# Performance work log

Measured on AMD Instinct MI355X. Metric: run time of the kernel, lower is better.

The kernel has to match this reference:

```python
import jax, jax.numpy as jnp
import numpy as np

EMBED = 1024
HEADS = 16
HEAD_DIM = EMBED // HEADS
EPS = 1e-5  # torch LayerNorm default


def setup_inputs() -> dict:
    key = jax.random.key(0)
    ks = jax.random.split(key, 11)
    s = 1.0 / np.sqrt(EMBED)
    def lin(kw, kb):
        W = jax.random.uniform(kw, (EMBED, EMBED), jnp.float32, -s, s)
        b = jax.random.uniform(kb, (EMBED,), jnp.float32, -s, s)
        return W, b
    Wq, bq = lin(ks[0], ks[1])
    Wk, bk = lin(ks[2], ks[3])
    Wv, bv = lin(ks[4], ks[5])
    Wo, bo = lin(ks[6], ks[7])
    x = jax.random.normal(ks[8], (2, 2048, EMBED), jnp.float32)
    gamma = jnp.ones((EMBED,), jnp.float32)
    beta = jnp.zeros((EMBED,), jnp.float32)
    return {"x": x, "Wq": Wq, "bq": bq, "Wk": Wk, "bk": bk,
            "Wv": Wv, "bv": bv, "Wo": Wo, "bo": bo,
            "gamma": gamma, "beta": beta}


def _attn(x, Wq, bq, Wk, bk, Wv, bv, Wo, bo, gamma, beta):
    N, S, _ = x.shape
    # torch Linear: y = x @ W.T + b
    q = (x @ Wq.T + bq).reshape(N, S, HEADS, HEAD_DIM).transpose(0, 2, 1, 3)
    k = (x @ Wk.T + bk).reshape(N, S, HEADS, HEAD_DIM).transpose(0, 2, 1, 3)
    v = (x @ Wv.T + bv).reshape(N, S, HEADS, HEAD_DIM).transpose(0, 2, 1, 3)
    energy = jnp.einsum("bhqd,bhkd->bhqk", q, k) / np.sqrt(HEAD_DIM)
    causal = jnp.tril(jnp.ones((S, S), bool))  # [S,S]
    energy = jnp.where(causal[None, None], energy, -jnp.inf)
    attn = jax.nn.softmax(energy, axis=-1)
    out = jnp.einsum("bhqk,bhkd->bhqd", attn, v)
    out = out.transpose(0, 2, 1, 3).reshape(N, S, EMBED)
    out = out @ Wo.T + bo
    # residual + LayerNorm
    h = out + x
    mu = jnp.mean(h, axis=-1, keepdims=True)
    var = jnp.var(h, axis=-1, keepdims=True)
    return (h - mu) * jax.lax.rsqrt(var + EPS) * gamma + beta


def reference(x, Wq, bq, Wk, bk, Wv, bv, Wo, bo, gamma, beta):
    return _attn(x, Wq, bq, Wk, bk, Wv, bv, Wo, bo, gamma, beta)
```

## Files before the change

kernel.cpp:

```cpp
#include <hip/hip_runtime.h>

typedef __attribute__((ext_vector_type(8))) short short8;
typedef __attribute__((ext_vector_type(4))) float f32x4;
typedef __attribute__((ext_vector_type(4))) short short4v;

__device__ __forceinline__ short f2bs(float f) {
    union { float f; unsigned u; } c; c.f = f;
    unsigned r = 0x7FFFu + ((c.u >> 16) & 1u);
    return (short)((c.u + r) >> 16);
}

__device__ __forceinline__ unsigned fbits(float f) {
    union { float f; unsigned u; } c; c.f = f; return c.u;
}

__device__ __forceinline__ float fast_exp2(float x) {
    float r;
    asm("v_exp_f32 %0, %1" : "=v"(r) : "v"(x));
    return r;
}

__device__ __forceinline__ void gld_lds16(const void* g, void* l) {
    __builtin_amdgcn_global_load_lds(
        (const __attribute__((address_space(1))) unsigned int*)g,
        (__attribute__((address_space(3))) unsigned int*)l, 16, 0, 0);
}

__device__ __forceinline__ f32x4 mfma16(short8 a, short8 b, f32x4 c) {
    return __builtin_amdgcn_mfma_f32_16x16x32_bf16(a, b, c, 0, 0, 0);
}

template<int N> __device__ __forceinline__ void vmwait() {
    if constexpr (N == 0)      asm volatile("s_waitcnt vmcnt(0)" ::: "memory");
    else if constexpr (N == 3) asm volatile("s_waitcnt vmcnt(3)" ::: "memory");
    else if constexpr (N == 4) asm volatile("s_waitcnt vmcnt(4)" ::: "memory");
}

__global__ __launch_bounds__(256) void cvtall_kernel(
    const float* __restrict__ x,
    const float* __restrict__ Wq, const float* __restrict__ Wk,
    const float* __restrict__ Wv, const float* __restrict__ Wo,
    short* __restrict__ xb, short* __restrict__ wqkv, short* __restrict__ wob)
{
    int i = blockIdx.x * 256 + threadIdx.x;
    const float* src; short* dst; int off;
    if (i < 1048576) { src = x; dst = xb; off = i; }
    else {
        int j = i - 1048576, which = j >> 18;
        off = j & 262143;
        src = which == 0 ? Wq : (which == 1 ? Wk : (which == 2 ? Wv : Wo));
        dst = which == 3 ? wob : (wqkv + (size_t)which * 1048576);
    }
    float4 v = ((const float4*)src)[off];
    short4v o;
    o.x = f2bs(v.x); o.y = f2bs(v.y); o.z = f2bs(v.z); o.w = f2bs(v.w);
    ((short4v*)dst)[off] = o;
}

#define BN 128
#define BK 32

template<int MODE, int BMt>
__global__ __launch_bounds__(256) void gemm_bt(
    const short* __restrict__ A, const short* __restrict__ B,
    int M, int N, int K,
    const float* __restrict__ b0, const float* __restrict__ b1, const float* __restrict__ b2,
    short* __restrict__ oq, short* __restrict__ ok_, short* __restrict__ ov,
    const float* __restrict__ bo, const float* __restrict__ xres,
    float* __restrict__ outf)
{
    constexpr int IM = BMt / 32;
    constexpr int BUFSZ = (BMt + BN) * BK;
    constexpr int LPS = (BMt == 128) ? 4 : 3;
    __shared__ __align__(16) short SM[3 * BUFSZ];
    const int tid = threadIdx.x;
    const int wave = tid >> 6, lane = tid & 63;
    const int lhi = lane >> 4, llo = lane & 15;
    const int row0 = blockIdx.x * BMt, col0 = blockIdx.y * BN;
    const int wr = (wave >> 1) * (BMt / 2), wc = (wave & 1) * 64;

    f32x4 acc[IM][4] = {};

    const short* gA0 = A + (size_t)(row0 + (tid >> 2)) * K + (tid & 3) * 8;
    const short* gA1 = A + (size_t)(row0 + 64 + (tid >> 2)) * K + (tid & 3) * 8;
    const short* gB0 = B + (size_t)(col0 + (tid >> 2)) * K + (tid & 3) * 8;
    const short* gB1 = B + (size_t)(col0 + 64 + (tid >> 2)) * K + (tid & 3) * 8;

    auto stage = [&](int kk, int bf) {
        short* As = SM + bf * BUFSZ;
        short* Bs = As + BMt * BK;
        gld_lds16(gA0 + kk, &As[wave * 512]);
        if constexpr (BMt == 128) gld_lds16(gA1 + kk, &As[2048 + wave * 512]);
        gld_lds16(gB0 + kk, &Bs[wave * 512]);
        gld_lds16(gB1 + kk, &Bs[2048 + wave * 512]);
    };

    const int NT = K / BK;
    stage(0, 0);
    stage(BK, 1);

    for (int kt = 0; kt < NT; ++kt) {
        if (kt < NT - 1) vmwait<LPS>(); else vmwait<0>();
        __builtin_amdgcn_s_barrier();
        __builtin_amdgcn_sched_barrier(0);
        if (kt + 2 < NT) stage((kt + 2) * BK, (kt + 2) % 3);
        const short* As = SM + (kt % 3) * BUFSZ;
        const short* Bs = As + BMt * BK;
        short8 af[IM], bfr[4];
        #pragma unroll
        for (int i = 0; i < IM; ++i)
            af[i] = *(const short8*)&As[(wr + i * 16 + llo) * BK + lhi * 8];
        #pragma unroll
        for (int j = 0; j < 4; ++j)
            bfr[j] = *(const short8*)&Bs[(wc + j * 16 + llo) * BK + lhi * 8];
        #pragma unroll
        for (int i = 0; i < IM; ++i)
            #pragma unroll
            for (int j = 0; j < 4; ++j)
                acc[i][j] = mfma16(af[i], bfr[j], acc[i][j]);
    }

    if constexpr (MODE == 0) {
        const int which = (int)blockIdx.y >> 3;
        if (which < 2) {
            const float* bia = which == 0 ? b0 : b1;
            short* dst = which == 0 ? oq : ok_;
            #pragma unroll
            for (int i = 0; i < IM; ++i)
                #pragma unroll
                for (int j = 0; j < 4; ++j)
                    #pragma unroll
                    for (int r = 0; r < 4; ++r) {
                        int m = row0 + wr + i * 16 + lhi * 4 + r;
                        int nn = (col0 & 1023) + wc + j * 16 + llo;
                        float v = acc[i][j][r] + bia[nn];
                        int h = nn >> 6, d = nn & 63;
                        int bb = m >> 11, s = m & 2047;
                        dst[((size_t)((bb * 16 + h) * 2048 + s)) * 64 + d] = f2bs(v);
                    }
        } else {
            __syncthreads();
            short* T = SM + wave * (64 * 26);
            const int nn0 = (col0 - 2048) + wc;
            const int h = nn0 >> 6;
            const int bb = row0 >> 11;
            const int s0 = (row0 & 2047) + wr;
            short* vdst = ov + ((size_t)(bb * 16 + h) * 64) * 2048;
            #pragma unroll
            for (int i = 0; i < IM; ++i) {
                #pragma unroll
                for (int j = 0; j < 4; ++j) {
                    const float bias = b2[nn0 + j * 16 + llo];
                    unsigned u01 = __builtin_amdgcn_perm(fbits(acc[i][j][1] + bias),
                                                         fbits(acc[i][j][0] + bias), 0x07060302u);
                    unsigned u23 = __builtin_amdgcn_perm(fbits(acc[i][j][3] + bias),
                                                         fbits(acc[i][j][2] + bias), 0x07060302u);
                    unsigned* Tw = (unsigned*)&T[(j * 16 + llo) * 26];
                    Tw[lhi * 2]     = u01;
                    Tw[lhi * 2 + 1] = u23;
                }
                short8 a0 = *(const short8*)&T[lane * 26];
                short8 a1 = *(const short8*)&T[lane * 26 + 8];
                *(short8*)&vdst[(size_t)lane * 2048 + s0 + i * 16]     = a0;
                *(short8*)&vdst[(size_t)lane * 2048 + s0 + i * 16 + 8] = a1;
            }
        }
    } else {
        #pragma unroll
        for (int i = 0; i < IM; ++i)
            #pragma unroll
            for (int j = 0; j < 4; ++j)
                #pragma unroll
                for (int r = 0; r < 4; ++r) {
                    int m = row0 + wr + i * 16 + lhi * 4 + r;
                    int n = col0 + wc + j * 16 + llo;
                    size_t idx = (size_t)m * N + n;
                    outf[idx] = acc[i][j][r] + bo[n] + xres[idx];
                }
    }
}

#define SCL 0.18033688011f

__global__ __launch_bounds__(256) void attn_kernel(
    const short* __restrict__ Q, const short* __restrict__ K,
    const short* __restrict__ Vt, short* __restrict__ O)
{
    const int id = blockIdx.x;
    const int bh = (id & 7) * 4 + (id >> 8);
    const int qt = 31 - ((id >> 3) & 31);
    const int q0 = qt * 64;
    const int nt = qt + 1;

    const short* Qb = Q  + (size_t)bh * 2048 * 64;
    const short* Kb = K  + (size_t)bh * 2048 * 64;
    const short* Vb = Vt + (size_t)bh * 64 * 2048;

    __shared__ __align__(16) short SMEM[4 * 4096];
    __shared__ float Lred[2][64];
    short* Ksb = SMEM;
    short* Vsb = SMEM + 2 * 4096;

    const int tid = threadIdx.x, wave = tid >> 6, lane = tid & 63;
    const int lhi = lane >> 4, llo = lane & 15;
    const int kh = wave >> 1, qh = wave & 1;

    auto scale8 = [](short8 a) {
        short8 r;
        #pragma unroll
        for (int i = 0; i < 8; ++i) {
            union { unsigned u; float f; } c; c.u = ((unsigned)(unsigned short)a[i]) << 16;
            r[i] = f2bs(c.f * SCL);
        }
        return r;
    };
    short8 qf[2][2];
    #pragma unroll
    for (int qs = 0; qs < 2; ++qs)
        #pragma unroll
        for (int h = 0; h < 2; ++h)
            qf[qs][h] = scale8(*(const short8*)&Qb[(size_t)(q0 + qh * 32 + qs * 16 + llo) * 64 + h * 32 + lhi * 8]);

    const int tr = tid >> 3, tc = tid & 7, sc = tc ^ (tr & 7);
    const short* kS0 = Kb + (size_t)tr * 64 + sc * 8;
    const short* kS1 = Kb + (size_t)(32 + tr) * 64 + sc * 8;
    const short* vS0 = Vb + (size_t)tr * 2048 + sc * 8;
    const short* vS1 = Vb + (size_t)(32 + tr) * 2048 + sc * 8;
    const int dOff = wave * 512;

    f32x4 o[4][2] = {};
    float lp[2] = {0.f, 0.f};

    gld_lds16(kS0, Ksb + dOff);
    gld_lds16(kS1, Ksb + 2048 + dOff);
    gld_lds16(vS0, Vsb + dOff);
    gld_lds16(vS1, Vsb + 2048 + dOff);
    __syncthreads();

    const int gbase = kh * 32 + ((llo & 12) << 1) + (llo & 3);
    const int vrow = 0;

    int cur = 0;
    for (int kt = 0; kt < nt; ++kt) {
        const int kk0 = kt * 64;
        if (kt + 1 < nt) {
            const int nk = kk0 + 64;
            gld_lds16(kS0 + (size_t)nk * 64, Ksb + (cur ^ 1) * 4096 + dOff);
            gld_lds16(kS1 + (size_t)nk * 64, Ksb + (cur ^ 1) * 4096 + 2048 + dOff);
            gld_lds16(vS0 + nk, Vsb + (cur ^ 1) * 4096 + dOff);
            gld_lds16(vS1 + nk, Vsb + (cur ^ 1) * 4096 + 2048 + dOff);
        }

        const short* Kc = Ksb + cur * 4096;
        const short* Vc = Vsb + cur * 4096;
        f32x4 st[2][2];
        __builtin_amdgcn_s_setprio(1);
        #pragma unroll
        for (int s = 0; s < 2; ++s) {
            const int g = gbase + s * 4;
            const int sw = (g & 7) << 3;
            short8 kf0 = *(const short8*)&Kc[g * 64 + ((lhi * 8) ^ sw)];
            short8 kf1 = *(const short8*)&Kc[g * 64 + ((lhi * 8 + 32) ^ sw)];
            #pragma unroll
            for (int qs = 0; qs < 2; ++qs) {
                f32x4 a = {};
                a = mfma16(kf0, qf[qs][0], a);
                st[s][qs] = mfma16(kf1, qf[qs][1], a);
            }
        }
        __builtin_amdgcn_s_setprio(0);

        if (kt == nt - 1) {
            #pragma unroll
            for (int s = 0; s < 2; ++s)
                #pragma unroll
                for (int qs = 0; qs < 2; ++qs)
                    #pragma unroll
                    for (int j = 0; j < 4; ++j)
                        if (kk0 + kh * 32 + lhi * 8 + s * 4 + j > q0 + qh * 32 + qs * 16 + llo)
                            st[s][qs][j] = -1e30f;
        }

        short8 pb[2];
        #pragma unroll
        for (int qs = 0; qs < 2; ++qs) {
            #pragma unroll
            for (int s = 0; s < 2; ++s)
                #pragma unroll
                for (int j = 0; j < 4; ++j) {
                    st[s][qs][j] = fast_exp2(st[s][qs][j]);
                    lp[qs] += st[s][qs][j];
                }
            union { short8 s8; unsigned u[4]; } pk;
            pk.u[0] = __builtin_amdgcn_perm(fbits(st[0][qs][1]), fbits(st[0][qs][0]), 0x07060302u);
            pk.u[1] = __builtin_amdgcn_perm(fbits(st[0][qs][3]), fbits(st[0][qs][2]), 0x07060302u);
            pk.u[2] = __builtin_amdgcn_perm(fbits(st[1][qs][1]), fbits(st[1][qs][0]), 0x07060302u);
            pk.u[3] = __builtin_amdgcn_perm(fbits(st[1][qs][3]), fbits(st[1][qs][2]), 0x07060302u);
            pb[qs] = pk.s8;
        }

        __builtin_amdgcn_s_setprio(1);
        #pragma unroll
        for (int ds = 0; ds < 4; ++ds) {
            const int row = ds * 16 + llo;
            const int sw = (row & 7) << 3;
            short8 vf = *(const short8*)&Vc[row * 64 + ((kh * 32 + lhi * 8) ^ sw)];
            o[ds][0] = mfma16(vf, pb[0], o[ds][0]);
            o[ds][1] = mfma16(vf, pb[1], o[ds][1]);
        }
        __builtin_amdgcn_s_setprio(0);

        if (kt + 1 < nt) __syncthreads();
        cur ^= 1;
    }

    #pragma unroll
    for (int qs = 0; qs < 2; ++qs) {
        float lq = lp[qs];
        lq += __shfl_xor(lq, 16);
        lq += __shfl_xor(lq, 32);
        if (lhi == 0) Lred[kh][qh * 32 + qs * 16 + llo] = lq;
    }
    __syncthreads();

    float* OredF = (float*)SMEM;
    #pragma unroll
    for (int ds = 0; ds < 4; ++ds)
        #pragma unroll
        for (int qs = 0; qs < 2; ++qs)
            #pragma unroll
            for (int r = 0; r < 4; ++r)
                OredF[kh * 4096 + (ds * 16 + lhi * 4 + r) * 64 + qh * 32 + qs * 16 + llo] = o[ds][qs][r];
    __syncthreads();

    const int b = bh >> 4, h = bh & 15;
    const int qq = tid >> 2, dg = tid & 3;
    const float linv = 1.f / (Lred[0][qq] + Lred[1][qq]);
    short vout[16];
    #pragma unroll
    for (int dd = 0; dd < 16; ++dd) {
        const int d = dg * 16 + dd;
        float v = OredF[d * 64 + qq] + OredF[4096 + d * 64 + qq];
        vout[dd] = f2bs(v * linv);
    }
    short* dst = O + ((size_t)(b * 2048 + q0 + qq)) * 1024 + h * 64 + dg * 16;
    *(short8*)dst       = *(short8*)&vout[0];
    *(short8*)(dst + 8) = *(short8*)&vout[8];
}

__global__ __launch_bounds__(256) void ln_kernel(float* __restrict__ out,
        const float* __restrict__ gamma, const float* __restrict__ beta)
{
    const int row = blockIdx.x;
    float* p = out + (size_t)row * 1024;
    const int tid = threadIdx.x;
    float4 v = ((const float4*)p)[tid];
    float s = v.x + v.y + v.z + v.w;
    float ss = v.x * v.x + v.y * v.y + v.z * v.z + v.w * v.w;
    #pragma unroll
    for (int d = 1; d < 64; d <<= 1) {
        s  += __shfl_xor(s, d);
        ss += __shfl_xor(ss, d);
    }
    __shared__ float red[8];
    const int wave = tid >> 6, lane = tid & 63;
    if (lane == 0) { red[wave] = s; red[4 + wave] = ss; }
    __syncthreads();
    s  = red[0] + red[1] + red[2] + red[3];
    ss = red[4] + red[5] + red[6] + red[7];
    const float mu = s * (1.0f / 1024.0f);
    const float var = ss * (1.0f / 1024.0f) - mu * mu;
    const float rstd = rsqrtf(var + 1e-5f);
    float4 g = ((const float4*)gamma)[tid];
    float4 b = ((const float4*)beta)[tid];
    v.x = (v.x - mu) * rstd * g.x + b.x;
    v.y = (v.y - mu) * rstd * g.y + b.y;
    v.z = (v.z - mu) * rstd * g.z + b.z;
    v.w = (v.w - mu) * rstd * g.w + b.w;
    ((float4*)p)[tid] = v;
}

extern "C" void kernel_launch(void* const* d_in, const int* in_sizes, int n_in,
                              void* d_out, int out_size, void* d_ws, size_t ws_size,
                              hipStream_t stream)
{
    const float* x  = (const float*)d_in[0];
    const float* Wq = (const float*)d_in[1];
    const float* bq = (const float*)d_in[2];
    const float* Wk = (const float*)d_in[3];
    const float* bk = (const float*)d_in[4];
    const float* Wv = (const float*)d_in[5];
    const float* bv = (const float*)d_in[6];
    const float* Wo = (const float*)d_in[7];
    const float* bo = (const float*)d_in[8];
    const float* gamma = (const float*)d_in[9];
    const float* beta  = (const float*)d_in[10];
    float* out = (float*)d_out;

    char* ws = (char*)d_ws;
    short* xb   = (short*)(ws);
    short* wqkv = (short*)(ws + (8ull  << 20));
    short* wob  = (short*)(ws + (14ull << 20));
    short* qb   = (short*)(ws + (16ull << 20));
    short* kb   = (short*)(ws + (24ull << 20));
    short* vtb  = (short*)(ws + (32ull << 20));
    short* ab   = xb;

    cvtall_kernel<<<8192, 256, 0, stream>>>(x, Wq, Wk, Wv, Wo, xb, wqkv, wob);

    gemm_bt<0, 128><<<dim3(32, 24), 256, 0, stream>>>(xb, wqkv, 4096, 3072, 1024,
        bq, bk, bv, qb, kb, vtb, nullptr, nullptr, nullptr);

    attn_kernel<<<1024, 256, 0, stream>>>(qb, kb, vtb, ab);

    gemm_bt<1, 64><<<dim3(64, 8), 256, 0, stream>>>(ab, wob, 4096, 1024, 1024,
        nullptr, nullptr, nullptr, nullptr, nullptr, nullptr, bo, x, out);

    ln_kernel<<<4096, 256, 0, stream>>>(out, gamma, beta);
}
```

Before: 119.6 us.

## Pair low and high causal query tiles per attention block for balance and K/V reuse

Each attention block now processes two query tiles, p and 31-p, so every block does the same amount of causal work, and the K/V tiles loaded for the first p+1 steps serve both. The grid is halved to 512 blocks. The P matrix now goes through a padded LDS buffer so the PV MFMA can take P as the A operand. The final reduction across the two key halves is rewritten to go through LDS with direct per-element stores. In exchange the kernel holds more registers (two Q fragment sets, two accumulators), uses more LDS, and has fewer blocks to cover the CUs.

```diff
diff --git a/kernel.cpp b/kernel.cpp
--- a/kernel.cpp
+++ b/kernel.cpp
@@ -3,6 +3,8 @@
 typedef __attribute__((ext_vector_type(8))) short short8;
 typedef __attribute__((ext_vector_type(4))) float f32x4;
 typedef __attribute__((ext_vector_type(4))) short short4v;
+
+template<bool B> struct BoolC { static constexpr bool value = B; };
 
 __device__ __forceinline__ short f2bs(float f) {
     union { float f; unsigned u; } c; c.f = f;
@@ -187,23 +189,28 @@
     const short* __restrict__ Vt, short* __restrict__ O)
 {
     const int id = blockIdx.x;
-    const int bh = (id & 7) * 4 + (id >> 8);
-    const int qt = 31 - ((id >> 3) & 31);
-    const int q0 = qt * 64;
-    const int nt = qt + 1;
+    const int u = id >> 3;
+    const int bh = (id & 7) * 4 + (u & 3);
+    const int s4 = u >> 2;
+    const int p = (s4 < 8) ? (2 * s4) : (31 - 2 * s4);
+    const int q0L = p * 64, q0H = (31 - p) * 64;
+    const int ntH = 32 - p;
 
     const short* Qb = Q  + (size_t)bh * 2048 * 64;
     const short* Kb = K  + (size_t)bh * 2048 * 64;
     const short* Vb = Vt + (size_t)bh * 64 * 2048;
 
     __shared__ __align__(16) short SMEM[4 * 4096];
+    __shared__ __align__(16) short Ps[2][2][32 * 68];
     __shared__ float Lred[2][64];
+
     short* Ksb = SMEM;
     short* Vsb = SMEM + 2 * 4096;
 
     const int tid = threadIdx.x, wave = tid >> 6, lane = tid & 63;
     const int lhi = lane >> 4, llo = lane & 15;
     const int kh = wave >> 1, qh = wave & 1;
+    const int khs = kh * 32;
 
     auto scale8 = [](short8 a) {
         short8 r;
@@ -214,12 +221,14 @@
         }
         return r;
     };
-    short8 qf[2][2];
+    short8 qfH[2][2], qfL[2][2];
     #pragma unroll
     for (int qs = 0; qs < 2; ++qs)
         #pragma unroll
-        for (int h = 0; h < 2; ++h)
-            qf[qs][h] = scale8(*(const short8*)&Qb[(size_t)(q0 + qh * 32 + qs * 16 + llo) * 64 + h * 32 + lhi * 8]);
+        for (int dh = 0; dh < 2; ++dh) {
+            qfH[qs][dh] = scale8(*(const short8*)&Qb[(size_t)(q0H + qh * 32 + qs * 16 + llo) * 64 + dh * 32 + lhi * 8]);
+            qfL[qs][dh] = scale8(*(const short8*)&Qb[(size_t)(q0L + qh * 32 + qs * 16 + llo) * 64 + dh * 32 + lhi * 8]);
+        }
 
     const int tr = tid >> 3, tc = tid & 7, sc = tc ^ (tr & 7);
     const short* kS0 = Kb + (size_t)tr * 64 + sc * 8;
@@ -228,8 +237,8 @@
     const short* vS1 = Vb + (size_t)(32 + tr) * 2048 + sc * 8;
     const int dOff = wave * 512;
 
-    f32x4 o[4][2] = {};
-    float lp[2] = {0.f, 0.f};
+    f32x4 oH[4][2] = {}, oL[4][2] = {};
+    float lpH[2] = {0.f, 0.f}, lpL[2] = {0.f, 0.f};
 
     gld_lds16(kS0, Ksb + dOff);
     gld_lds16(kS1, Ksb + 2048 + dOff);
@@ -237,115 +246,149 @@
     gld_lds16(vS1, Vsb + 2048 + dOff);
     __syncthreads();
 
-    const int gbase = kh * 32 + ((llo & 12) << 1) + (llo & 3);
-    const int vrow = 0;
+    const int swq = (llo & 7) << 3;
 
     int cur = 0;
-    for (int kt = 0; kt < nt; ++kt) {
+    auto tile = [&](int kt, auto dualc) {
+        constexpr bool DUAL = decltype(dualc)::value;
         const int kk0 = kt * 64;
-        if (kt + 1 < nt) {
+        if (kt + 1 < ntH) {
             const int nk = kk0 + 64;
             gld_lds16(kS0 + (size_t)nk * 64, Ksb + (cur ^ 1) * 4096 + dOff);
             gld_lds16(kS1 + (size_t)nk * 64, Ksb + (cur ^ 1) * 4096 + 2048 + dOff);
             gld_lds16(vS0 + nk, Vsb + (cur ^ 1) * 4096 + dOff);
             gld_lds16(vS1 + nk, Vsb + (cur ^ 1) * 4096 + 2048 + dOff);
         }
-
         const short* Kc = Ksb + cur * 4096;
         const short* Vc = Vsb + cur * 4096;
-        f32x4 st[2][2];
+
+        f32x4 stH[2][2], stL[2][2];
         __builtin_amdgcn_s_setprio(1);
         #pragma unroll
-        for (int s = 0; s < 2; ++s) {
-            const int g = gbase + s * 4;
-            const int sw = (g & 7) << 3;
-            short8 kf0 = *(const short8*)&Kc[g * 64 + ((lhi * 8) ^ sw)];
-            short8 kf1 = *(const short8*)&Kc[g * 64 + ((lhi * 8 + 32) ^ sw)];
+        for (int t = 0; t < 2; ++t) {
+            const int row = khs + t * 16 + llo;
+            short8 kf0 = *(const short8*)&Kc[row * 64 + ((lhi * 8) ^ swq)];
+            short8 kf1 = *(const short8*)&Kc[row * 64 + ((lhi * 8 + 32) ^ swq)];
             #pragma unroll
             for (int qs = 0; qs < 2; ++qs) {
                 f32x4 a = {};
-                a = mfma16(kf0, qf[qs][0], a);
-                st[s][qs] = mfma16(kf1, qf[qs][1], a);
+                a = mfma16(kf0, qfH[qs][0], a);
+                stH[t][qs] = mfma16(kf1, qfH[qs][1], a);
+                if (DUAL) {
+                    f32x4 bb = {};
+                    bb = mfma16(kf0, qfL[qs][0], bb);
+                    stL[t][qs] = mfma16(kf1, qfL[qs][1], bb);
+                }
             }
         }
         __builtin_amdgcn_s_setprio(0);
 
-        if (kt == nt - 1) {
-            #pragma unroll
-            for (int s = 0; s < 2; ++s)
-                #pragma unroll
-                for (int qs = 0; qs < 2; ++qs)
+        auto smx2 = [&](f32x4 (&st)[2][2], float (&lp)[2], int qg0, int HLi, bool diag) {
+            if (diag) {
+                #pragma unroll
+                for (int t = 0; t < 2; ++t)
                     #pragma unroll
-                    for (int j = 0; j < 4; ++j)
-                        if (kk0 + kh * 32 + lhi * 8 + s * 4 + j > q0 + qh * 32 + qs * 16 + llo)
-                            st[s][qs][j] = -1e30f;
-        }
-
-        short8 pb[2];
-        #pragma unroll
-        for (int qs = 0; qs < 2; ++qs) {
-            #pragma unroll
-            for (int s = 0; s < 2; ++s)
-                #pragma unroll
-                for (int j = 0; j < 4; ++j) {
-                    st[s][qs][j] = fast_exp2(st[s][qs][j]);
-                    lp[qs] += st[s][qs][j];
-                }
-            union { short8 s8; unsigned u[4]; } pk;
-            pk.u[0] = __builtin_amdgcn_perm(fbits(st[0][qs][1]), fbits(st[0][qs][0]), 0x07060302u);
-            pk.u[1] = __builtin_amdgcn_perm(fbits(st[0][qs][3]), fbits(st[0][qs][2]), 0x07060302u);
-            pk.u[2] = __builtin_amdgcn_perm(fbits(st[1][qs][1]), fbits(st[1][qs][0]), 0x07060302u);
-            pk.u[3] = __builtin_amdgcn_perm(fbits(st[1][qs][3]), fbits(st[1][qs][2]), 0x07060302u);
-            pb[qs] = pk.s8;
-        }
-
+                    for (int qs = 0; qs < 2; ++qs)
+                        #pragma unroll
+                        for (int j = 0; j < 4; ++j)
+                            if (kk0 + khs + t * 16 + lhi * 4 + j > qg0 + qs * 16 + llo)
+                                st[t][qs][j] = -1e30f;
+            }
+            unsigned* Pw = (unsigned*)Ps[qh][HLi];
+            #pragma unroll
+            for (int qs = 0; qs < 2; ++qs) {
+                float rs = 0.f;
+                #pragma unroll
+                for (int t = 0; t < 2; ++t)
+                    #pragma unroll
+                    for (int j = 0; j < 4; ++j) {
+                        st[t][qs][j] = fast_exp2(st[t][qs][j]);
+                        rs += st[t][qs][j];
+                    }
+                lp[qs] += rs;
+                const int base = (qs * 16 + llo) * 34 + kh * 16 + lhi * 2;
+                Pw[base]          = __builtin_amdgcn_perm(fbits(st[0][qs][1]), fbits(st[0][qs][0]), 0x07060302u);
+                Pw[base + 1]      = __builtin_amdgcn_perm(fbits(st[0][qs][3]), fbits(st[0][qs][2]), 0x07060302u);
+                Pw[base + 8]      = __builtin_amdgcn_perm(fbits(st[1][qs][1]), fbits(st[1][qs][0]), 0x07060302u);
+                Pw[base + 9]      = __builtin_amdgcn_perm(fbits(st[1][qs][3]), fbits(st[1][qs][2]), 0x07060302u);
+            }
+        };
+        smx2(stH, lpH, q0H + qh * 32, 0, kt == ntH - 1);
+        if (DUAL) smx2(stL, lpL, q0L + qh * 32, 1, kt == p);
+
+        short8 pfH[2], pfL[2];
+        #pragma unroll
+        for (int qs = 0; qs < 2; ++qs)
+            pfH[qs] = *(const short8*)&Ps[qh][0][(qs * 16 + llo) * 68 + khs + lhi * 8];
+        if (DUAL)
+            #pragma unroll
+            for (int qs = 0; qs < 2; ++qs)
+                pfL[qs] = *(const short8*)&Ps[qh][1][(qs * 16 + llo) * 68 + khs + lhi * 8];
         __builtin_amdgcn_s_setprio(1);
         #pragma unroll
-        for (int ds = 0; ds < 4; ++ds) {
-            const int row = ds * 16 + llo;
-            const int sw = (row & 7) << 3;
-            short8 vf = *(const short8*)&Vc[row * 64 + ((kh * 32 + lhi * 8) ^ sw)];
-            o[ds][0] = mfma16(vf, pb[0], o[ds][0]);
-            o[ds][1] = mfma16(vf, pb[1], o[ds][1]);
+        for (int dt = 0; dt < 4; ++dt) {
+            const int row = dt * 16 + llo;
+            short8 vf = *(const short8*)&Vc[row * 64 + ((khs + lhi * 8) ^ swq)];
+            oH[dt][0] = mfma16(pfH[0], vf, oH[dt][0]);
+            oH[dt][1] = mfma16(pfH[1], vf, oH[dt][1]);
+            if (DUAL) {
+                oL[dt][0] = mfma16(pfL[0], vf, oL[dt][0]);
+                oL[dt][1] = mfma16(pfL[1], vf, oL[dt][1]);
+            }
         }
         __builtin_amdgcn_s_setprio(0);
 
-        if (kt + 1 < nt) __syncthreads();
+        if (kt + 1 < ntH) __syncthreads();
         cur ^= 1;
-    }
+    };
+
+    for (int kt = 0; kt <= p; ++kt)      tile(kt, BoolC<true>{});
+    for (int kt = p + 1; kt < ntH; ++kt) tile(kt, BoolC<false>{});
 
     #pragma unroll
     for (int qs = 0; qs < 2; ++qs) {
-        float lq = lp[qs];
-        lq += __shfl_xor(lq, 16);
-        lq += __shfl_xor(lq, 32);
-        if (lhi == 0) Lred[kh][qh * 32 + qs * 16 + llo] = lq;
+        lpH[qs] += __shfl_xor(lpH[qs], 16); lpH[qs] += __shfl_xor(lpH[qs], 32);
+        lpL[qs] += __shfl_xor(lpL[qs], 16); lpL[qs] += __shfl_xor(lpL[qs], 32);
     }
     __syncthreads();
 
-    float* OredF = (float*)SMEM;
-    #pragma unroll
-    for (int ds = 0; ds < 4; ++ds)
-        #pragma unroll
-        for (int qs = 0; qs < 2; ++qs)
-            #pragma unroll
-            for (int r = 0; r < 4; ++r)
-                OredF[kh * 4096 + (ds * 16 + lhi * 4 + r) * 64 + qh * 32 + qs * 16 + llo] = o[ds][qs][r];
-    __syncthreads();
-
+    float* F = (float*)SMEM;
     const int b = bh >> 4, h = bh & 15;
-    const int qq = tid >> 2, dg = tid & 3;
-    const float linv = 1.f / (Lred[0][qq] + Lred[1][qq]);
-    short vout[16];
-    #pragma unroll
-    for (int dd = 0; dd < 16; ++dd) {
-        const int d = dg * 16 + dd;
-        float v = OredF[d * 64 + qq] + OredF[4096 + d * 64 + qq];
-        vout[dd] = f2bs(v * linv);
-    }
-    short* dst = O + ((size_t)(b * 2048 + q0 + qq)) * 1024 + h * 64 + dg * 16;
-    *(short8*)dst       = *(short8*)&vout[0];
-    *(short8*)(dst + 8) = *(short8*)&vout[8];
+
+    auto finalize = [&](f32x4 (&o)[4][2], float (&lp)[2], int q0X, int HLi) {
+        if (kh == 1) {
+            #pragma unroll
+            for (int qs = 0; qs < 2; ++qs) {
+                if (lhi == 0) Lred[HLi][qh * 32 + qs * 16 + llo] = lp[qs];
+                #pragma unroll
+                for (int dt = 0; dt < 4; ++dt)
+                    #pragma unroll
+                    for (int r = 0; r < 4; ++r)
+                        F[(qh * 32 + qs * 16 + lhi * 4 + r) * 65 + dt * 16 + llo] = o[dt][qs][r];
+            }
+        }
+        __syncthreads();
+        if (kh == 0) {
+            #pragma unroll
+            for (int qs = 0; qs < 2; ++qs) {
+                const float inv = 1.f / (lp[qs] + Lred[HLi][qh * 32 + qs * 16 + llo]);
+                #pragma unroll
+                for (int r = 0; r < 4; ++r) {
+                    const float iv = __shfl(inv, lhi * 4 + r);
+                    const int qp = qh * 32 + qs * 16 + lhi * 4 + r;
+                    const size_t rowO = (size_t)(b * 2048 + q0X + qp) * 1024 + h * 64;
+                    #pragma unroll
+                    for (int dt = 0; dt < 4; ++dt) {
+                        const int d = dt * 16 + llo;
+                        O[rowO + d] = f2bs((o[dt][qs][r] + F[qp * 65 + d]) * iv);
+                    }
+                }
+            }
+        }
+        __syncthreads();
+    };
+    finalize(oH, lpH, q0H, 0);
+    finalize(oL, lpL, q0L, 1);
 }
 
 __global__ __launch_bounds__(256) void ln_kernel(float* __restrict__ out,
@@ -411,7 +454,7 @@
     gemm_bt<0, 128><<<dim3(32, 24), 256, 0, stream>>>(xb, wqkv, 4096, 3072, 1024,
         bq, bk, bv, qb, kb, vtb, nullptr, nullptr, nullptr);
 
-    attn_kernel<<<1024, 256, 0, stream>>>(qb, kb, vtb, ab);
+    attn_kernel<<<512, 256, 0, stream>>>(qb, kb, vtb, ab);
 
     gemm_bt<1, 64><<<dim3(64, 8), 256, 0, stream>>>(ab, wob, 4096, 1024, 1024,
         nullptr, nullptr, nullptr, nullptr, nullptr, nullptr, bo, x, out);
```

Result: faster. 112.7 us (-5.8%).
